# Performance work log

Hardware: AMD Instinct MI355X
Metric: run time of the kernel (lower is better)

Reference implementation:

```python
import jax, jax.numpy as jnp
import numpy as np

N, IN, HID, OUT, E, G = 20000, 256, 256, 128, 320000, 64


def setup_inputs() -> dict:
    key = jax.random.key(0)
    ks = jax.random.split(key, 16)
    s = 0.05
    x = jax.random.normal(ks[0], (N, IN), jnp.float32)
    edge_index = jax.random.randint(ks[1], (2, E), 0, N, dtype=jnp.int32)
    batch = jnp.sort(jax.random.randint(ks[2], (N,), 0, G, dtype=jnp.int32))
    return {
        "x": x,
        "edge_index": edge_index,
        "batch": batch,
        "num_graphs": G,
        "W1": jax.random.normal(ks[3], (HID, IN), jnp.float32) * s,
        "b1": jnp.zeros((HID,), jnp.float32),
        "W2": jax.random.normal(ks[4], (HID, HID), jnp.float32) * s,
        "b2": jnp.zeros((HID,), jnp.float32),
        "W3": jax.random.normal(ks[5], (HID, HID), jnp.float32) * s,
        "b3": jnp.zeros((HID,), jnp.float32),
        "W4": jax.random.normal(ks[6], (OUT, HID), jnp.float32) * s,
        "b4": jnp.zeros((OUT,), jnp.float32),
        "lin_w": jax.random.normal(ks[7], (1, OUT), jnp.float32) * s,
        "lin_b": jnp.zeros((1,), jnp.float32),
    }


def reference(x, edge_index, batch, num_graphs, W1, b1, W2, b2, W3, b3, W4, b4, lin_w, lin_b):
    row, col = edge_index[0], edge_index[1]
    n = x.shape[0]
    # degree-based symmetric-ish norm (as in source: degree of row only)
    deg = jax.ops.segment_sum(jnp.ones((row.shape[0],), x.dtype), row, num_segments=n)
    deg_inv_sqrt = deg ** -0.5  # 0-degree -> inf, matching torch deg.pow(-0.5)
    norm = (deg_inv_sqrt[row] * deg_inv_sqrt[col])[:, None]  # [E,1]

    def gcn_layer(h, W, b):
        h = h @ W.T + b                                  # dense linear [N,out]
        msgs = norm * h[row]                             # gather + scale [E,out]
        return jax.ops.segment_sum(msgs, col, num_segments=n)  # scatter-add

    h = gcn_layer(x, W1, b1)
    h = gcn_layer(h, W2, b2)
    h = gcn_layer(h, W3, b3)
    h = gcn_layer(h, W4, b4)

    # to_dense_batch(...).mean(dim=1): sum per graph / max graph size (padded mean)
    sums = jax.ops.segment_sum(h, batch, num_segments=num_graphs)          # [G,OUT]
    counts = jax.ops.segment_sum(jnp.ones((n,), h.dtype), batch, num_segments=num_graphs)
    x_new = sums / jnp.max(counts)
    return x_new @ lin_w.T + lin_b  # [G,1]
```

## Files before the change

kernel.cpp:

```cpp
#include <hip/hip_runtime.h>
#include <math.h>

#define NN      20000
#define IN_DIM  256
#define HID_DIM 256
#define OUT_DIM 128
#define EE      320000
#define GG      64

#define P_H     8
#define CHUNK   (EE / P_H)
#define NW      10000
#define PSTRIDE 10240
#define MGB     20
#define SB      1250
#define GB      313


__device__ __forceinline__ float ldf_mall(const float* p) {
  return __hip_atomic_load(p, __ATOMIC_RELAXED, __HIP_MEMORY_SCOPE_AGENT);
}
__device__ __forceinline__ int ldi_mall(const int* p) {
  return __hip_atomic_load(p, __ATOMIC_RELAXED, __HIP_MEMORY_SCOPE_AGENT);
}

__global__ __launch_bounds__(1024) void k_hist_chain(
    const int* __restrict__ erow, const int* __restrict__ ecol,
    unsigned int* __restrict__ pdeg, unsigned int* __restrict__ pccnt,
    const float* __restrict__ W1, const float* __restrict__ b1,
    const float* __restrict__ W2, const float* __restrict__ b2,
    const float* __restrict__ W3, const float* __restrict__ b3,
    const float* __restrict__ W4, const float* __restrict__ b4,
    const float* __restrict__ lw, float* __restrict__ q1g,
    float* __restrict__ dv) {
  __shared__ __align__(16) char smem[40960];
  const int bid = blockIdx.x, tid = threadIdx.x;

  if (bid < 2 * P_H) {
    unsigned int* h = (unsigned int*)smem;
    const int  p    = (bid < P_H) ? bid : bid - P_H;
    const int* src  = (bid < P_H) ? erow : ecol;
    unsigned int* slab = ((bid < P_H) ? pdeg : pccnt) + (size_t)p * PSTRIDE;
    for (int w = tid; w < NW; w += 1024) h[w] = 0u;
    __syncthreads();
    const int base = p * CHUNK;
    for (int i = tid; i < CHUNK; i += 1024) {
      int v = src[base + i];
      atomicAdd(&h[v >> 1], 1u << ((v & 1) << 4));
    }
    __syncthreads();
    for (int w = tid; w < NW; w += 1024) slab[w] = h[w];
    return;
  }

  float* fs   = (float*)smem;
  float* lws  = fs;
  float* qa   = fs + 128;
  float* qb   = fs + 384;
  float* qc   = fs + 640;
  float* qd   = fs + 896;
  float* part = fs + 1152;
  float* red  = fs + 5248;
  const int jj = tid & 63, tq = tid >> 6;

  if (tid < 128) lws[tid] = lw[tid];
  __syncthreads();

  auto gemv = [&](const float* W, const float* qin, float* qout, int K) {
    const int tl = K >> 4, t0 = tq * tl;
    float ax = 0.f, ay = 0.f, az = 0.f, aw = 0.f;
#pragma unroll 8
    for (int t = t0; t < t0 + tl; ++t) {
      const float4 wv = *(const float4*)(W + (size_t)t * 256 + jj * 4);
      const float qv = qin[t];
      ax += wv.x * qv; ay += wv.y * qv; az += wv.z * qv; aw += wv.w * qv;
    }
    part[(tq * 64 + jj) * 4 + 0] = ax; part[(tq * 64 + jj) * 4 + 1] = ay;
    part[(tq * 64 + jj) * 4 + 2] = az; part[(tq * 64 + jj) * 4 + 3] = aw;
    __syncthreads();
    if (tid < 256) {
      float s = 0.f;
#pragma unroll
      for (int k = 0; k < 16; ++k) s += part[(k * 64 + (tid >> 2)) * 4 + (tid & 3)];
      qout[tid] = s;
    }
    __syncthreads();
  };

  gemv(W4, lws, qa, OUT_DIM);
  gemv(W3, qa, qb, HID_DIM);
  gemv(W2, qb, qc, HID_DIM);
  gemv(W1, qc, qd, HID_DIM);
  if (tid < 256) q1g[tid] = qd[tid];

  auto dot = [&](const float* a, const float* bl, int K, float* dst) {
    float p = (tid < K) ? a[tid] * bl[tid] : 0.f;
#pragma unroll
    for (int off = 32; off; off >>= 1) p += __shfl_down(p, off);
    if ((tid & 63) == 0) red[tid >> 6] = p;
    __syncthreads();
    if (tid == 0) { float s = 0.f; for (int k = 0; k < 16; ++k) s += red[k]; *dst = s; }
    __syncthreads();
  };
  dot(b1, qc, HID_DIM, &dv[0]);
  dot(b2, qb, HID_DIM, &dv[1]);
  dot(b3, qa, HID_DIM, &dv[2]);
  dot(b4, lws, OUT_DIM, &dv[3]);
}

__global__ __launch_bounds__(1024) void k_msc_mv(
    const unsigned int* __restrict__ pdeg, const unsigned int* __restrict__ pccnt,
    int* __restrict__ deg, int* __restrict__ ccnt, int* __restrict__ mergedone,
    int* __restrict__ cstart, int* __restrict__ cursor,
    const int* __restrict__ batch, float* __restrict__ outcnt,
    const float* __restrict__ x, const float* __restrict__ q1,
    float* __restrict__ u0) {
  int bid = blockIdx.x, tid = threadIdx.x, lane = tid & 63, wid = tid >> 6;

  if (bid == 0) {
    if (tid == 0) {
      while (__hip_atomic_load(mergedone, __ATOMIC_RELAXED, __HIP_MEMORY_SCOPE_AGENT) < MGB)
        __builtin_amdgcn_s_sleep(1);
      (void)__hip_atomic_load(mergedone, __ATOMIC_ACQUIRE, __HIP_MEMORY_SCOPE_AGENT);
    }
    __syncthreads();
    __shared__ int ws[16];
    const int PER = 20;
    int base = tid * PER;
    int v[PER]; int sum = 0;
#pragma unroll
    for (int i = 0; i < PER; ++i) {
      int idx = base + i;
      v[i] = (idx < NN) ? ldi_mall(&ccnt[idx]) : 0;
      sum += v[i];
    }
    int incl = sum;
#pragma unroll
    for (int off = 1; off < 64; off <<= 1) { int t = __shfl_up(incl, off); if (lane >= off) incl += t; }
    if (lane == 63) ws[wid] = incl;
    __syncthreads();
    if (tid == 0) { int r = 0; for (int j = 0; j < 16; ++j) { int t = ws[j]; ws[j] = r; r += t; } }
    __syncthreads();
    int run = ws[wid] + incl - sum;
#pragma unroll
    for (int i = 0; i < PER; ++i) {
      int idx = base + i;
      if (idx < NN) { cstart[idx] = run; cursor[idx] = run; }
      run += v[i];
    }
    if (tid == 1023) cstart[NN] = run;
    return;
  }

  if (bid <= MGB) {
    int w0 = (bid - 1) * 500;
    for (int w = w0 + tid; w < w0 + 500; w += 1024) {
      unsigned int dlo = 0, dhi = 0, clo = 0, chi = 0;
#pragma unroll
      for (int p = 0; p < P_H; ++p) {
        unsigned int ud = pdeg[(size_t)p * PSTRIDE + w];
        unsigned int uc = pccnt[(size_t)p * PSTRIDE + w];
        dlo += ud & 0xFFFFu; dhi += ud >> 16;
        clo += uc & 0xFFFFu; chi += uc >> 16;
      }
      deg[2 * w] = (int)dlo; deg[2 * w + 1] = (int)dhi;
      atomicAdd(&ccnt[2 * w], (int)clo);
      atomicAdd(&ccnt[2 * w + 1], (int)chi);
    }
    __syncthreads();
    if (tid == 0)
      __hip_atomic_fetch_add(mergedone, 1, __ATOMIC_RELEASE, __HIP_MEMORY_SCOPE_AGENT);
    return;
  }

  if (bid == MGB + 1) {
    for (int base = 0; base < NN; base += 1024) {
      int n = base + tid;
      int b = -1; float cn = 0.f;
      if (n < NN) { b = batch[n]; cn = 1.f; }
#pragma unroll
      for (int off = 1; off < 64; off <<= 1) {
        float c2 = __shfl_up(cn, off);
        int   b2 = __shfl_up(b, off);
        if (lane >= off && b2 == b) cn += c2;
      }
      int bn = __shfl_down(b, 1);
      if (((lane == 63) || (bn != b)) && b >= 0) atomicAdd(&outcnt[b], cn);
    }
    return;
  }

  int r = (bid - (MGB + 2)) * 16 + wid;
  if (r >= NN) return;
  const float4 xv = *(const float4*)(x + (size_t)r * IN_DIM + lane * 4);
  const float4 qv = *(const float4*)(q1 + lane * 4);
  float s = xv.x * qv.x + xv.y * qv.y + xv.z * qv.z + xv.w * qv.w;
#pragma unroll
  for (int off = 32; off; off >>= 1) s += __shfl_down(s, off);
  if (lane == 0) u0[r] = s;
}

__global__ __launch_bounds__(256) void k_scatter(
    const int* __restrict__ erow, const int* __restrict__ ecol,
    const int* __restrict__ deg, int* __restrict__ cursor,
    int2* __restrict__ sedge) {
  int e = blockIdx.x * 256 + threadIdx.x;
  int r = erow[e], c = ecol[e];
  int slot = atomicAdd(&cursor[c], 1);
  float dr = (float)deg[r], dc = (float)deg[c];
  float val = (1.0f / sqrtf(dr)) * (1.0f / sqrtf(dc));
  sedge[slot] = make_int2(r, __float_as_int(val));
}

__global__ __launch_bounds__(256) void k_gather(
    const int* __restrict__ cstart, const int2* __restrict__ sedge,
    const float* __restrict__ uin, const float* __restrict__ dptr,
    float* __restrict__ uout) {
  int gid = blockIdx.x * 256 + threadIdx.x;
  int n = gid >> 2, l = gid & 3;
  if (n >= NN) return;
  int s0 = cstart[n], s1 = cstart[n + 1];
  float acc = 0.f, es = 0.f;
  for (int s = s0 + l; s < s1; s += 4) {
    int2 ev = sedge[s];
    float v = __int_as_float(ev.y);
    acc += v * uin[ev.x];
    es  += v;
  }
  acc += __shfl_xor(acc, 1); es += __shfl_xor(es, 1);
  acc += __shfl_xor(acc, 2); es += __shfl_xor(es, 2);
  if (l == 0) uout[n] = acc + dptr[0] * es;
}

__global__ __launch_bounds__(256) void k_gather_pool_final(
    const int* __restrict__ cstart, const int2* __restrict__ sedge,
    const float* __restrict__ uin, const float* __restrict__ dptr,
    const int* __restrict__ batch, float* __restrict__ outsum,
    const float* __restrict__ outcnt, const float* __restrict__ lb,
    float* __restrict__ out, int* __restrict__ done, int nblocks) {
  int gid = blockIdx.x * 256 + threadIdx.x;
  int lane = threadIdx.x & 63;
  int n = gid >> 2, l = gid & 3;
  float pv = 0.f; int b = -1;
  if (n < NN) {
    int s0 = cstart[n], s1 = cstart[n + 1];
    float acc = 0.f, es = 0.f;
    for (int s = s0 + l; s < s1; s += 4) {
      int2 ev = sedge[s];
      float v = __int_as_float(ev.y);
      acc += v * uin[ev.x];
      es  += v;
    }
    acc += __shfl_xor(acc, 1); es += __shfl_xor(es, 1);
    acc += __shfl_xor(acc, 2); es += __shfl_xor(es, 2);
    b = batch[n];
    if (l == 0) pv = acc + dptr[0] * es;
  }
#pragma unroll
  for (int off = 1; off < 64; off <<= 1) {
    float s2 = __shfl_up(pv, off);
    int   b2 = __shfl_up(b, off);
    if (lane >= off && b2 == b) pv += s2;
  }
  int bn = __shfl_down(b, 1);
  if (((lane == 63) || (bn != b)) && b >= 0) atomicAdd(&outsum[b], pv);

  __syncthreads();
  __shared__ int winner;
  if (threadIdx.x == 0) {
    int old = __hip_atomic_fetch_add(done, 1, __ATOMIC_RELAXED, __HIP_MEMORY_SCOPE_AGENT);
    winner = (old == nblocks - 1) ? 1 : 0;
  }
  __syncthreads();
  if (winner && threadIdx.x < GG) {
    int g = threadIdx.x;
    float m = ldf_mall(&outcnt[g]);
#pragma unroll
    for (int off = 32; off; off >>= 1) m = fmaxf(m, __shfl_xor(m, off));
    out[g] = ldf_mall(&outsum[g]) / m + lb[0];
  }
}

extern "C" void kernel_launch(void* const* d_in, const int* in_sizes, int n_in,
                              void* d_out, int out_size, void* d_ws, size_t ws_size,
                              hipStream_t stream) {
  (void)in_sizes; (void)n_in; (void)out_size; (void)ws_size;
  const float* x     = (const float*)d_in[0];
  const int*   erow  = (const int*)d_in[1];
  const int*   ecol  = ((const int*)d_in[1]) + EE;
  const int*   batch = (const int*)d_in[2];
  const float* W1 = (const float*)d_in[4];
  const float* b1 = (const float*)d_in[5];
  const float* W2 = (const float*)d_in[6];
  const float* b2 = (const float*)d_in[7];
  const float* W3 = (const float*)d_in[8];
  const float* b3 = (const float*)d_in[9];
  const float* W4 = (const float*)d_in[10];
  const float* b4 = (const float*)d_in[11];
  const float* lw = (const float*)d_in[12];
  const float* lb = (const float*)d_in[13];
  float* out = (float*)d_out;

  const size_t PN = 80128;
  char* w = (char*)d_ws;
  int*   ccnt      = (int*)w;    w += PN;
  float* outsum    = (float*)w;  w += 256;
  float* outcnt    = (float*)w;  w += 256;
  int*   done      = (int*)w;    w += 256;
  int*   mergedone = (int*)w;    w += 256;
  size_t zbytes = (size_t)(w - (char*)d_ws);
  int*   deg    = (int*)w;    w += PN;
  int*   cstart = (int*)w;    w += PN + 256;
  int*   cursor = (int*)w;    w += PN;
  int2*  sedge  = (int2*)w;   w += (size_t)EE * 8;
  unsigned int* pdeg  = (unsigned int*)w; w += (size_t)P_H * PSTRIDE * 4;
  unsigned int* pccnt = (unsigned int*)w; w += (size_t)P_H * PSTRIDE * 4;
  float* q1     = (float*)w;  w += 1024;
  float* dv     = (float*)w;  w += 256;
  float* u0     = (float*)w;  w += PN;
  float* u1     = (float*)w;  w += PN;
  float* u2     = (float*)w;  w += PN;
  float* u3     = (float*)w;  w += PN;

  hipMemsetAsync(d_ws, 0, zbytes, stream);
  k_hist_chain<<<2 * P_H + 1, 1024, 0, stream>>>(erow, ecol, pdeg, pccnt,
                                                 W1, b1, W2, b2, W3, b3, W4, b4,
                                                 lw, q1, dv);
  k_msc_mv<<<MGB + 2 + 1250, 1024, 0, stream>>>(pdeg, pccnt, deg, ccnt, mergedone,
                                                cstart, cursor, batch, outcnt,
                                                x, q1, u0);
  k_scatter<<<SB, 256, 0, stream>>>(erow, ecol, deg, cursor, sedge);
  k_gather<<<GB, 256, 0, stream>>>(cstart, sedge, u0, dv + 0, u1);
  k_gather<<<GB, 256, 0, stream>>>(cstart, sedge, u1, dv + 1, u2);
  k_gather<<<GB, 256, 0, stream>>>(cstart, sedge, u2, dv + 2, u3);
  k_gather_pool_final<<<GB, 256, 0, stream>>>(cstart, sedge, u3, dv + 3, batch,
                                              outsum, outcnt, lb, out, done, GB);
}
```

Measured before the change: 96.22 us.

## Deterministic CSR slots from histogram ranks; split weight-chain GEMV across 16 blocks

The column histogram now records each edge's within-chunk rank and the merge step stores per-chunk prefix offsets, so the scatter computes its destination slot directly instead of taking a global atomic cursor. The serial single-block GEMV chain is spread over 16 blocks that meet at grid-wide counter barriers between stages. This removes contended atomics in the scatter and shortens the chain's critical path, at the cost of extra rank/offset arrays in memory and spin barriers that assume all blocks are co-resident.

```diff
diff --git a/kernel.cpp b/kernel.cpp
--- a/kernel.cpp
+++ b/kernel.cpp
@@ -12,6 +12,7 @@
 #define CHUNK   (EE / P_H)
 #define NW      10000
 #define PSTRIDE 10240
+#define CHB     16
 #define MGB     20
 #define SB      1250
 #define GB      313
@@ -27,91 +28,110 @@
 __global__ __launch_bounds__(1024) void k_hist_chain(
     const int* __restrict__ erow, const int* __restrict__ ecol,
     unsigned int* __restrict__ pdeg, unsigned int* __restrict__ pccnt,
+    unsigned short* __restrict__ rankb,
     const float* __restrict__ W1, const float* __restrict__ b1,
     const float* __restrict__ W2, const float* __restrict__ b2,
     const float* __restrict__ W3, const float* __restrict__ b3,
     const float* __restrict__ W4, const float* __restrict__ b4,
-    const float* __restrict__ lw, float* __restrict__ q1g,
-    float* __restrict__ dv) {
+    const float* __restrict__ lw,
+    float* __restrict__ q4g, float* __restrict__ q3g,
+    float* __restrict__ q2g, float* __restrict__ q1g,
+    float* __restrict__ dv, int* __restrict__ chaindone) {
   __shared__ __align__(16) char smem[40960];
   const int bid = blockIdx.x, tid = threadIdx.x;
 
   if (bid < 2 * P_H) {
     unsigned int* h = (unsigned int*)smem;
-    const int  p    = (bid < P_H) ? bid : bid - P_H;
-    const int* src  = (bid < P_H) ? erow : ecol;
-    unsigned int* slab = ((bid < P_H) ? pdeg : pccnt) + (size_t)p * PSTRIDE;
+    const int  p   = bid & (P_H - 1);
+    const bool isc = bid >= P_H;
+    const int* src = isc ? ecol : erow;
+    unsigned int* slab = (isc ? pccnt : pdeg) + (size_t)p * PSTRIDE;
     for (int w = tid; w < NW; w += 1024) h[w] = 0u;
     __syncthreads();
     const int base = p * CHUNK;
     for (int i = tid; i < CHUNK; i += 1024) {
       int v = src[base + i];
-      atomicAdd(&h[v >> 1], 1u << ((v & 1) << 4));
+      int sh = (v & 1) << 4;
+      unsigned int old = atomicAdd(&h[v >> 1], 1u << sh);
+      if (isc) rankb[base + i] = (unsigned short)((old >> sh) & 0xFFFFu);
     }
     __syncthreads();
     for (int w = tid; w < NW; w += 1024) slab[w] = h[w];
     return;
   }
 
-  float* fs   = (float*)smem;
-  float* lws  = fs;
-  float* qa   = fs + 128;
-  float* qb   = fs + 384;
-  float* qc   = fs + 640;
-  float* qd   = fs + 896;
-  float* part = fs + 1152;
-  float* red  = fs + 5248;
-  const int jj = tid & 63, tq = tid >> 6;
-
-  if (tid < 128) lws[tid] = lw[tid];
+  const int cb = bid - 2 * P_H;
+  float* fs  = (float*)smem;
+  float* lwl = fs;
+  float* qs4 = fs + 128;
+  float* qs3 = fs + 384;
+  float* qs2 = fs + 640;
+  float* part = fs + 896;
+  float* red  = fs + 1920;
+  const int jj = tid & 15, tt = tid >> 4;
+  const int jg = cb * 16 + jj;
+
+  if (tid < 128) lwl[tid] = lw[tid];
   __syncthreads();
 
-  auto gemv = [&](const float* W, const float* qin, float* qout, int K) {
-    const int tl = K >> 4, t0 = tq * tl;
-    float ax = 0.f, ay = 0.f, az = 0.f, aw = 0.f;
-#pragma unroll 8
-    for (int t = t0; t < t0 + tl; ++t) {
-      const float4 wv = *(const float4*)(W + (size_t)t * 256 + jj * 4);
-      const float qv = qin[t];
-      ax += wv.x * qv; ay += wv.y * qv; az += wv.z * qv; aw += wv.w * qv;
-    }
-    part[(tq * 64 + jj) * 4 + 0] = ax; part[(tq * 64 + jj) * 4 + 1] = ay;
-    part[(tq * 64 + jj) * 4 + 2] = az; part[(tq * 64 + jj) * 4 + 3] = aw;
-    __syncthreads();
-    if (tid < 256) {
+  auto arrive_wait = [&](int target) {
+    __syncthreads();
+    if (tid == 0) {
+      __hip_atomic_fetch_add(chaindone, 1, __ATOMIC_RELEASE, __HIP_MEMORY_SCOPE_AGENT);
+      while (__hip_atomic_load(chaindone, __ATOMIC_RELAXED, __HIP_MEMORY_SCOPE_AGENT) < target)
+        __builtin_amdgcn_s_sleep(1);
+      (void)__hip_atomic_load(chaindone, __ATOMIC_ACQUIRE, __HIP_MEMORY_SCOPE_AGENT);
+    }
+    __syncthreads();
+  };
+  auto stage = [&](const float* W, const float* qin, int K, float* qout_g) {
+    float acc = 0.f;
+    for (int t = tt; t < K; t += 64) acc += W[(size_t)t * 256 + jg] * qin[t];
+    part[tt * 16 + jj] = acc;
+    __syncthreads();
+    if (tid < 16) {
       float s = 0.f;
 #pragma unroll
-      for (int k = 0; k < 16; ++k) s += part[(k * 64 + (tid >> 2)) * 4 + (tid & 3)];
-      qout[tid] = s;
-    }
-    __syncthreads();
+      for (int k = 0; k < 64; ++k) s += part[k * 16 + tid];
+      qout_g[cb * 16 + tid] = s;
+    }
   };
-
-  gemv(W4, lws, qa, OUT_DIM);
-  gemv(W3, qa, qb, HID_DIM);
-  gemv(W2, qb, qc, HID_DIM);
-  gemv(W1, qc, qd, HID_DIM);
-  if (tid < 256) q1g[tid] = qd[tid];
-
-  auto dot = [&](const float* a, const float* bl, int K, float* dst) {
-    float p = (tid < K) ? a[tid] * bl[tid] : 0.f;
-#pragma unroll
-    for (int off = 32; off; off >>= 1) p += __shfl_down(p, off);
-    if ((tid & 63) == 0) red[tid >> 6] = p;
-    __syncthreads();
-    if (tid == 0) { float s = 0.f; for (int k = 0; k < 16; ++k) s += red[k]; *dst = s; }
+  auto load_q = [&](const float* qg, float* qdst) {
+    if (tid < 256) qdst[tid] = ldf_mall(qg + tid);
     __syncthreads();
   };
-  dot(b1, qc, HID_DIM, &dv[0]);
-  dot(b2, qb, HID_DIM, &dv[1]);
-  dot(b3, qa, HID_DIM, &dv[2]);
-  dot(b4, lws, OUT_DIM, &dv[3]);
+
+  stage(W4, lwl, OUT_DIM, q4g);  arrive_wait(1 * CHB);
+  load_q(q4g, qs4);
+  stage(W3, qs4, HID_DIM, q3g);  arrive_wait(2 * CHB);
+  load_q(q3g, qs3);
+  stage(W2, qs3, HID_DIM, q2g);  arrive_wait(3 * CHB);
+  load_q(q2g, qs2);
+  stage(W1, qs2, HID_DIM, q1g);
+
+  if (cb == 0) {
+    __syncthreads();
+    auto dot = [&](const float* a, const float* bl, int K, float* dst) {
+      float p = (tid < K) ? a[tid] * bl[tid] : 0.f;
+#pragma unroll
+      for (int off = 32; off; off >>= 1) p += __shfl_down(p, off);
+      if ((tid & 63) == 0) red[tid >> 6] = p;
+      __syncthreads();
+      if (tid == 0) { float s = 0.f; for (int k = 0; k < 16; ++k) s += red[k]; *dst = s; }
+      __syncthreads();
+    };
+    dot(b1, qs2, HID_DIM, &dv[0]);
+    dot(b2, qs3, HID_DIM, &dv[1]);
+    dot(b3, qs4, HID_DIM, &dv[2]);
+    dot(b4, lwl, OUT_DIM, &dv[3]);
+  }
 }
 
 __global__ __launch_bounds__(1024) void k_msc_mv(
     const unsigned int* __restrict__ pdeg, const unsigned int* __restrict__ pccnt,
-    int* __restrict__ deg, int* __restrict__ ccnt, int* __restrict__ mergedone,
-    int* __restrict__ cstart, int* __restrict__ cursor,
+    int* __restrict__ deg, int* __restrict__ ccnt,
+    unsigned short* __restrict__ chunkoff, int* __restrict__ mergedone,
+    int* __restrict__ cstart,
     const int* __restrict__ batch, float* __restrict__ outcnt,
     const float* __restrict__ x, const float* __restrict__ q1,
     float* __restrict__ u0) {
@@ -145,7 +165,7 @@
 #pragma unroll
     for (int i = 0; i < PER; ++i) {
       int idx = base + i;
-      if (idx < NN) { cstart[idx] = run; cursor[idx] = run; }
+      if (idx < NN) cstart[idx] = run;
       run += v[i];
     }
     if (tid == 1023) cstart[NN] = run;
@@ -156,16 +176,18 @@
     int w0 = (bid - 1) * 500;
     for (int w = w0 + tid; w < w0 + 500; w += 1024) {
       unsigned int dlo = 0, dhi = 0, clo = 0, chi = 0;
+      const int c0 = 2 * w, c1 = 2 * w + 1;
 #pragma unroll
       for (int p = 0; p < P_H; ++p) {
         unsigned int ud = pdeg[(size_t)p * PSTRIDE + w];
         unsigned int uc = pccnt[(size_t)p * PSTRIDE + w];
         dlo += ud & 0xFFFFu; dhi += ud >> 16;
+        chunkoff[(size_t)c0 * P_H + p] = (unsigned short)clo;
+        chunkoff[(size_t)c1 * P_H + p] = (unsigned short)chi;
         clo += uc & 0xFFFFu; chi += uc >> 16;
       }
-      deg[2 * w] = (int)dlo; deg[2 * w + 1] = (int)dhi;
-      atomicAdd(&ccnt[2 * w], (int)clo);
-      atomicAdd(&ccnt[2 * w + 1], (int)chi);
+      deg[c0]  = (int)dlo; deg[c1]  = (int)dhi;
+      ccnt[c0] = (int)clo; ccnt[c1] = (int)chi;
     }
     __syncthreads();
     if (tid == 0)
@@ -202,11 +224,14 @@
 
 __global__ __launch_bounds__(256) void k_scatter(
     const int* __restrict__ erow, const int* __restrict__ ecol,
-    const int* __restrict__ deg, int* __restrict__ cursor,
+    const int* __restrict__ deg, const int* __restrict__ cstart,
+    const unsigned short* __restrict__ chunkoff,
+    const unsigned short* __restrict__ rankb,
     int2* __restrict__ sedge) {
   int e = blockIdx.x * 256 + threadIdx.x;
   int r = erow[e], c = ecol[e];
-  int slot = atomicAdd(&cursor[c], 1);
+  int p = e / CHUNK;
+  int slot = cstart[c] + (int)chunkoff[(size_t)c * P_H + p] + (int)rankb[e];
   float dr = (float)deg[r], dc = (float)deg[c];
   float val = (1.0f / sqrtf(dr)) * (1.0f / sqrtf(dc));
   sedge[slot] = make_int2(r, __float_as_int(val));
@@ -303,33 +328,38 @@
 
   const size_t PN = 80128;
   char* w = (char*)d_ws;
-  int*   ccnt      = (int*)w;    w += PN;
   float* outsum    = (float*)w;  w += 256;
   float* outcnt    = (float*)w;  w += 256;
   int*   done      = (int*)w;    w += 256;
   int*   mergedone = (int*)w;    w += 256;
+  int*   chaindone = (int*)w;    w += 256;
   size_t zbytes = (size_t)(w - (char*)d_ws);
   int*   deg    = (int*)w;    w += PN;
+  int*   ccnt   = (int*)w;    w += PN;
   int*   cstart = (int*)w;    w += PN + 256;
-  int*   cursor = (int*)w;    w += PN;
   int2*  sedge  = (int2*)w;   w += (size_t)EE * 8;
-  unsigned int* pdeg  = (unsigned int*)w; w += (size_t)P_H * PSTRIDE * 4;
-  unsigned int* pccnt = (unsigned int*)w; w += (size_t)P_H * PSTRIDE * 4;
-  float* q1     = (float*)w;  w += 1024;
-  float* dv     = (float*)w;  w += 256;
-  float* u0     = (float*)w;  w += PN;
-  float* u1     = (float*)w;  w += PN;
-  float* u2     = (float*)w;  w += PN;
-  float* u3     = (float*)w;  w += PN;
+  unsigned int*   pdeg  = (unsigned int*)w;   w += (size_t)P_H * PSTRIDE * 4;
+  unsigned int*   pccnt = (unsigned int*)w;   w += (size_t)P_H * PSTRIDE * 4;
+  unsigned short* chunkoff = (unsigned short*)w; w += (size_t)NN * P_H * 2;
+  unsigned short* rankb    = (unsigned short*)w; w += (size_t)EE * 2;
+  float* q4 = (float*)w;  w += 1024;
+  float* q3 = (float*)w;  w += 1024;
+  float* q2 = (float*)w;  w += 1024;
+  float* q1 = (float*)w;  w += 1024;
+  float* dv = (float*)w;  w += 256;
+  float* u0 = (float*)w;  w += PN;
+  float* u1 = (float*)w;  w += PN;
+  float* u2 = (float*)w;  w += PN;
+  float* u3 = (float*)w;  w += PN;
 
   hipMemsetAsync(d_ws, 0, zbytes, stream);
-  k_hist_chain<<<2 * P_H + 1, 1024, 0, stream>>>(erow, ecol, pdeg, pccnt,
-                                                 W1, b1, W2, b2, W3, b3, W4, b4,
-                                                 lw, q1, dv);
-  k_msc_mv<<<MGB + 2 + 1250, 1024, 0, stream>>>(pdeg, pccnt, deg, ccnt, mergedone,
-                                                cstart, cursor, batch, outcnt,
+  k_hist_chain<<<2 * P_H + CHB, 1024, 0, stream>>>(erow, ecol, pdeg, pccnt, rankb,
+                                                   W1, b1, W2, b2, W3, b3, W4, b4,
+                                                   lw, q4, q3, q2, q1, dv, chaindone);
+  k_msc_mv<<<MGB + 2 + 1250, 1024, 0, stream>>>(pdeg, pccnt, deg, ccnt, chunkoff,
+                                                mergedone, cstart, batch, outcnt,
                                                 x, q1, u0);
-  k_scatter<<<SB, 256, 0, stream>>>(erow, ecol, deg, cursor, sedge);
+  k_scatter<<<SB, 256, 0, stream>>>(erow, ecol, deg, cstart, chunkoff, rankb, sedge);
   k_gather<<<GB, 256, 0, stream>>>(cstart, sedge, u0, dv + 0, u1);
   k_gather<<<GB, 256, 0, stream>>>(cstart, sedge, u1, dv + 1, u2);
   k_gather<<<GB, 256, 0, stream>>>(cstart, sedge, u2, dv + 2, u3);
```

After: 82.41 us. 14.4% less time.
